# Kernel optimization log

Measured on AMD Instinct MI355X. Metric: run time of the kernel, lower is better.

Reference implementation:

```python
import jax, jax.numpy as jnp
import numpy as np

B, N, E, L = 64, 50000, 1600000, 20
BN_EPS = 1e-5


def setup_inputs() -> dict:
    key = jax.random.key(0)
    ks = jax.random.split(key, 8)
    x = jax.random.normal(ks[0], (B, N), dtype=jnp.float32)
    edge_index = jax.random.randint(ks[1], (2, E), 0, N, dtype=jnp.int32)
    alpha = jax.random.normal(ks[2], (E,), dtype=jnp.float32)
    bias = jax.random.normal(ks[3], (E,), dtype=jnp.float32)
    # LazyLinear(num_labels) on [B, N] features
    W = jax.random.normal(ks[4], (L, N), dtype=jnp.float32) / np.sqrt(N)
    b_lin = jax.random.normal(ks[5], (L,), dtype=jnp.float32) * 0.01
    # LazyBatchNorm1d affine params over N features
    gamma = jnp.ones((N,), dtype=jnp.float32)
    beta = jnp.zeros((N,), dtype=jnp.float32)
    return {"x": x, "edge_index": edge_index, "alpha": alpha, "bias": bias,
            "W": W, "b_lin": b_lin, "gamma": gamma, "beta": beta}


def reference(x, edge_index, alpha, bias, W, b_lin, gamma, beta):
    src, dst = edge_index[0], edge_index[1]
    # gather per-edge source features and apply per-edge affine: [B, E]
    x_e = alpha * x[:, src] + bias
    # scatter-mean into destination nodes: [B, N]
    sums = jnp.zeros((x.shape[0], N), dtype=x.dtype).at[:, dst].add(x_e)
    counts = jnp.zeros((N,), dtype=x.dtype).at[dst].add(1.0)
    x_hat = sums / jnp.maximum(counts, 1.0)
    out = jnp.tanh(x_hat)
    # linear head: [B, L]
    pred = x_hat @ W.T + b_lin
    # BatchNorm1d (training mode: batch stats, biased variance)
    mu = jnp.mean(out, axis=0)
    var = jnp.var(out, axis=0)
    bn = (out - mu) / jnp.sqrt(var + BN_EPS) * gamma + beta
    return (pred, bn)
```

## Files before the change

kernel.cpp:

```cpp
#include <hip/hip_runtime.h>
#include <math.h>

#define NB 64
#define NL 20
#define BN_EPS 1e-5f

#define BIN_W 32
#define NBIN 1563
#define BIN_CAP 1280
#define CHUNK 4096

#define NSB 49
#define NSBP 64
#define CAP1 36864
#define NSLICE 9

__device__ __forceinline__ unsigned short f2bf(float f) {
    unsigned u = __float_as_uint(f);
    unsigned r = u + 0x7fff + ((u >> 16) & 1);
    return (unsigned short)(r >> 16);
}

__global__ __launch_bounds__(1024) void stage_kernel(
    const float* __restrict__ x, unsigned short* __restrict__ xTb,
    const int* __restrict__ src, const int* __restrict__ dst,
    const float* __restrict__ alpha, const float* __restrict__ bias,
    int* __restrict__ cnt1, uint2* __restrict__ buf1, int E, int Nn, int nA) {
    __shared__ unsigned hist[NSBP];
    __shared__ unsigned gbase[NSBP];
    __shared__ float tile[64][65];

    int tid = threadIdx.x;

    if ((int)blockIdx.x < nA) {
        int e0 = blockIdx.x * CHUNK;
        if (tid < NSBP) hist[tid] = 0;
        __syncthreads();

        uint2 pay[4];
        unsigned rk[4];
        int sb[4];
        #pragma unroll
        for (int k = 0; k < 4; ++k) {
            int e = e0 + k * 1024 + tid;
            sb[k] = -1;
            if (e < E) {
                int d = dst[e];
                int b = d >> 5;
                int dl = d & 31;
                pay[k].x = (unsigned)src[e] | ((unsigned)f2bf(alpha[e]) << 16);
                pay[k].y = (unsigned)f2bf(bias[e]) | ((unsigned)dl << 16) |
                           ((unsigned)b << 21);
                sb[k] = d >> 10;
                rk[k] = atomicAdd(&hist[sb[k]], 1u);
            }
        }
        __syncthreads();

        if (tid < NSBP) {
            unsigned v = hist[tid];
            if (v > 0) gbase[tid] = (unsigned)atomicAdd(&cnt1[tid], (int)v);
        }
        __syncthreads();

        #pragma unroll
        for (int k = 0; k < 4; ++k) {
            if (sb[k] >= 0) {
                unsigned di = gbase[sb[k]] + rk[k];
                if (di < CAP1)
                    buf1[(size_t)sb[k] * CAP1 + di] = pay[k];
            }
        }
    } else {
        int n0 = ((int)blockIdx.x - nA) * 64;
        int ln = tid & 63;
        int wv = tid >> 6;
        for (int r = wv; r < 64; r += 16) {
            int col = n0 + ln;
            tile[r][ln] = (col < Nn) ? x[r * Nn + col] : 0.f;
        }
        __syncthreads();
        for (int r = wv; r < 64; r += 16) {
            int node = n0 + r;
            if (node < Nn) xTb[(size_t)node * 64 + ln] = f2bf(tile[ln][r]);
        }
    }
}

__global__ __launch_bounds__(1024) void binB_kernel(
    const int* __restrict__ cnt1, const uint2* __restrict__ buf1,
    int* __restrict__ cursor, uint2* __restrict__ paybins) {
    __shared__ unsigned hist[32];
    __shared__ unsigned gbase[32];

    int tid = threadIdx.x;
    int sb = blockIdx.x / NSLICE;
    int slice = blockIdx.x % NSLICE;

    int lim = cnt1[sb];
    if (lim > CAP1) lim = CAP1;
    int cc = lim - slice * 4096;
    if (cc < 0) cc = 0;
    if (cc > 4096) cc = 4096;
    const uint2* pb = buf1 + (size_t)sb * CAP1 + (size_t)slice * 4096;

    if (tid < 32) hist[tid] = 0;
    __syncthreads();

    uint2 pay[4];
    unsigned rk[4];
    int lb[4];
    #pragma unroll
    for (int k = 0; k < 4; ++k) {
        int i = k * 1024 + tid;
        lb[k] = -1;
        if (i < cc) {
            pay[k] = pb[i];
            lb[k] = (int)((pay[k].y >> 21) & 31u);
            rk[k] = atomicAdd(&hist[lb[k]], 1u);
        }
    }
    __syncthreads();

    if (tid < 32) {
        unsigned v = hist[tid];
        if (v > 0)
            gbase[tid] = (unsigned)atomicAdd(&cursor[sb * 32 + tid], (int)v);
    }
    __syncthreads();

    #pragma unroll
    for (int k = 0; k < 4; ++k) {
        if (lb[k] >= 0) {
            int bin = sb * 32 + lb[k];
            unsigned di = gbase[lb[k]] + rk[k];
            if (di < BIN_CAP)
                paybins[(size_t)bin * BIN_CAP + di] = pay[k];
        }
    }
}

__global__ __launch_bounds__(256) void pull_fin4_kernel(
    const int* __restrict__ cursor, const uint2* __restrict__ paybins,
    const unsigned short* __restrict__ xTb, const float* __restrict__ W,
    const float* __restrict__ gamma, const float* __restrict__ beta,
    float* __restrict__ pred_part, float* __restrict__ bn, int Nn) {
    __shared__ __align__(16) char smem[16896];
    uint2* ed = (uint2*)smem;
    float (*xh)[66] = (float (*)[66])smem;
    float (*th)[66] = (float (*)[66])(smem + 8448);

    __shared__ float wl[NL][32];
    __shared__ unsigned h2[32], b2[32], c2[32];
    __shared__ float mu_s[32], a_s[32], be_s[32];

    const unsigned* xTbu = (const unsigned*)xTb;

    int bin = blockIdx.x;
    int tid = threadIdx.x;
    int ln = tid & 63;
    int w = tid >> 6;
    int n0 = bin * 32;
    int pair = ln >> 5;
    int h = ln & 31;

    int cnt = cursor[bin];
    if (cnt > BIN_CAP) cnt = BIN_CAP;
    const uint2* pb = paybins + (size_t)bin * BIN_CAP;

    for (int i = tid; i < NL * 32; i += 256) {
        int l = i >> 5, j = i & 31;
        wl[l][j] = (n0 + j < Nn) ? W[l * Nn + n0 + j] : 0.f;
    }
    if (tid < 32) { h2[tid] = 0; c2[tid] = 0; }
    __syncthreads();

    uint2 pA = {0, 0}, pB = {0, 0}, pC = {0, 0}, pD = {0, 0}, pE = {0, 0};
    {
        int i;
        i = tid;
        if (i < cnt) { pA = pb[i]; atomicAdd(&h2[(pA.y >> 16) & 31], 1u); }
        i = tid + 256;
        if (i < cnt) { pB = pb[i]; atomicAdd(&h2[(pB.y >> 16) & 31], 1u); }
        i = tid + 512;
        if (i < cnt) { pC = pb[i]; atomicAdd(&h2[(pC.y >> 16) & 31], 1u); }
        i = tid + 768;
        if (i < cnt) { pD = pb[i]; atomicAdd(&h2[(pD.y >> 16) & 31], 1u); }
        i = tid + 1024;
        if (i < cnt) { pE = pb[i]; atomicAdd(&h2[(pE.y >> 16) & 31], 1u); }
    }
    __syncthreads();

    if (tid < 32) {
        unsigned v = h2[tid];
        unsigned incl = v;
        #pragma unroll
        for (int off = 1; off < 32; off <<= 1) {
            unsigned t = __shfl_up(incl, off, 64);
            if (tid >= off) incl += t;
        }
        b2[tid] = incl - v;
    }
    __syncthreads();

    {
        if (tid < cnt) {
            unsigned dl = (pA.y >> 16) & 31;
            ed[b2[dl] + atomicAdd(&c2[dl], 1u)] = pA;
        }
        if (tid + 256 < cnt) {
            unsigned dl = (pB.y >> 16) & 31;
            ed[b2[dl] + atomicAdd(&c2[dl], 1u)] = pB;
        }
        if (tid + 512 < cnt) {
            unsigned dl = (pC.y >> 16) & 31;
            ed[b2[dl] + atomicAdd(&c2[dl], 1u)] = pC;
        }
        if (tid + 768 < cnt) {
            unsigned dl = (pD.y >> 16) & 31;
            ed[b2[dl] + atomicAdd(&c2[dl], 1u)] = pD;
        }
        if (tid + 1024 < cnt) {
            unsigned dl = (pE.y >> 16) & 31;
            ed[b2[dl] + atomicAdd(&c2[dl], 1u)] = pE;
        }
    }
    __syncthreads();

    float xv_reg[8], tv_reg[8];
    #pragma unroll
    for (int k = 0; k < 8; ++k) {
        int dl = w * 8 + k;
        int node = n0 + dl;
        int n = (int)h2[dl];
        unsigned bs = b2[dl];
        float accL0 = 0.f, accH0 = 0.f, accL1 = 0.f, accH1 = 0.f;
        float bs0 = 0.f, bs1 = 0.f;
        int j = 0;
        for (; j + 3 < n; j += 4) {
            uint2 e0 = ed[bs + j + pair];
            uint2 e1 = ed[bs + j + 2 + pair];
            unsigned v0 = xTbu[(size_t)(e0.x & 0xffffu) * 32 + h];
            unsigned v1 = xTbu[(size_t)(e1.x & 0xffffu) * 32 + h];
            float al0 = __uint_as_float(e0.x & 0xffff0000u);
            float al1 = __uint_as_float(e1.x & 0xffff0000u);
            bs0 += __uint_as_float((e0.y & 0xffffu) << 16);
            bs1 += __uint_as_float((e1.y & 0xffffu) << 16);
            accL0 = fmaf(al0, __uint_as_float(v0 << 16), accL0);
            accH0 = fmaf(al0, __uint_as_float(v0 & 0xffff0000u), accH0);
            accL1 = fmaf(al1, __uint_as_float(v1 << 16), accL1);
            accH1 = fmaf(al1, __uint_as_float(v1 & 0xffff0000u), accH1);
        }
        for (; j < n; j += 2) {
            int idx = j + pair;
            bool act = idx < n;
            uint2 e0 = ed[act ? (bs + idx) : bs];
            float al0 = act ? __uint_as_float(e0.x & 0xffff0000u) : 0.f;
            float bi0 = act ? __uint_as_float((e0.y & 0xffffu) << 16) : 0.f;
            unsigned v0 = xTbu[(size_t)(e0.x & 0xffffu) * 32 + h];
            bs0 += bi0;
            accL0 = fmaf(al0, __uint_as_float(v0 << 16), accL0);
            accH0 = fmaf(al0, __uint_as_float(v0 & 0xffff0000u), accH0);
        }
        float accL = accL0 + accL1;
        float accH = accH0 + accH1;
        float bsum = bs0 + bs1;
        accL += __shfl_xor(accL, 32, 64);
        accH += __shfl_xor(accH, 32, 64);
        bsum += __shfl_xor(bsum, 32, 64);
        float inv = 1.0f / fmaxf((float)n, 1.0f);
        float xlo = (accL + bsum) * inv;
        float xhi = (accH + bsum) * inv;
        float xv = pair ? xhi : xlo;
        float tv = tanhf(xv);
        xv_reg[k] = xv;
        tv_reg[k] = tv;

        float s = tv, q = tv * tv;
        #pragma unroll
        for (int off = 32; off > 0; off >>= 1) {
            s += __shfl_xor(s, off, 64);
            q += __shfl_xor(q, off, 64);
        }
        if (ln == 0) {
            float mu = s * (1.0f / 64.0f);
            float var = fmaxf(q * (1.0f / 64.0f) - mu * mu, 0.f);
            float invs = rsqrtf(var + BN_EPS);
            float gm = 1.f, bt = 0.f;
            if (node < Nn) { gm = gamma[node]; bt = beta[node]; }
            mu_s[dl] = mu;
            a_s[dl] = invs * gm;
            be_s[dl] = bt;
        }
    }
    __syncthreads();

    {
        int col = 2 * h + pair;
        #pragma unroll
        for (int k = 0; k < 8; ++k) {
            xh[w * 8 + k][col] = xv_reg[k];
            th[w * 8 + k][col] = tv_reg[k];
        }
    }
    __syncthreads();

    {
        float acc[5] = {0.f, 0.f, 0.f, 0.f, 0.f};
        for (int n = 0; n < 32; ++n) {
            float xv = xh[n][ln];
            #pragma unroll
            for (int k = 0; k < 5; ++k)
                acc[k] = fmaf(xv, wl[w + k * 4][n], acc[k]);
        }
        #pragma unroll
        for (int k = 0; k < 5; ++k)
            pred_part[(size_t)bin * (NB * NL) + ln * NL + (w + k * 4)] = acc[k];
    }

    for (int idx = tid; idx < 32 * 64; idx += 256) {
        int noff = idx & 31, bb = idx >> 5;
        int node = n0 + noff;
        if (node < Nn)
            bn[bb * Nn + node] =
                fmaf(th[noff][bb] - mu_s[noff], a_s[noff], be_s[noff]);
    }
}

__global__ __launch_bounds__(256) void reduce_pred_kernel(
    const float* __restrict__ part, const float* __restrict__ b_lin,
    float* __restrict__ pred, int nblk) {
    int out = blockIdx.x * 4 + (threadIdx.x >> 6);
    if (out >= NB * NL) return;
    int ln = threadIdx.x & 63;
    float s = 0.f;
    for (int i = ln; i < nblk; i += 64)
        s += part[(size_t)i * (NB * NL) + out];
    #pragma unroll
    for (int off = 32; off > 0; off >>= 1)
        s += __shfl_xor(s, off, 64);
    if (ln == 0) pred[out] = b_lin[out % NL] + s;
}

extern "C" void kernel_launch(void* const* d_in, const int* in_sizes, int n_in,
                              void* d_out, int out_size, void* d_ws, size_t ws_size,
                              hipStream_t stream) {
    const float* x     = (const float*)d_in[0];
    const int*   ei    = (const int*)d_in[1];
    const float* alpha = (const float*)d_in[2];
    const float* bias  = (const float*)d_in[3];
    const float* W     = (const float*)d_in[4];
    const float* b_lin = (const float*)d_in[5];
    const float* gamma = (const float*)d_in[6];
    const float* beta  = (const float*)d_in[7];

    const int Nn = in_sizes[0] / NB;
    const int E  = in_sizes[1] / 2;
    const int* src = ei;
    const int* dst = ei + E;

    const int ntile = (Nn + 63) / 64;
    const int nA    = (E + CHUNK - 1) / CHUNK;

    uint2*          paybins = (uint2*)d_ws;
    uint2*          buf1    = paybins + (size_t)NBIN * BIN_CAP;
    float*          pred_part = (float*)buf1;
    unsigned short* xTb     = (unsigned short*)(buf1 + (size_t)NSB * CAP1);
    int*            cnt1    = (int*)(xTb + (size_t)Nn * 64);
    int*            cursor  = cnt1 + NSBP;

    float* pred = (float*)d_out;
    float* bn   = pred + NB * NL;

    hipMemsetAsync(cnt1, 0, (NSBP + NBIN + 32) * sizeof(int), stream);

    stage_kernel<<<nA + ntile, 1024, 0, stream>>>(
        x, xTb, src, dst, alpha, bias, cnt1, buf1, E, Nn, nA);
    binB_kernel<<<NSB * NSLICE, 1024, 0, stream>>>(cnt1, buf1, cursor, paybins);
    pull_fin4_kernel<<<NBIN, 256, 0, stream>>>(cursor, paybins, xTb, W,
                                               gamma, beta, pred_part, bn, Nn);
    reduce_pred_kernel<<<(NB * NL + 3) / 4, 256, 0, stream>>>(
        pred_part, b_lin, pred, NBIN);
}
```

Before: 188.9 us.

## Halve destination bin width to 16 nodes and split pred reduction in two stages

Destination bins shrink from 32 to 16 nodes, which doubles the number of pull blocks (3125) and halves each block's shared memory and edge load, so more blocks can be resident and the gather latency is spread more evenly. The bin index encoding and binB local histogram widen to 64 sub-bins per superbin to match. Because the larger number of per-bin partial pred rows makes the final reduction longer, it becomes a two-stage reduction (128 blocks, then a final pass). Bounds checks on node < Nn are dropped, which relies on N being a multiple of 16. The per-bin capacity of 640 makes overflow drops more likely if a bin is denser than expected.

```diff
diff --git a/kernel.cpp b/kernel.cpp
--- a/kernel.cpp
+++ b/kernel.cpp
@@ -5,15 +5,18 @@
 #define NL 20
 #define BN_EPS 1e-5f
 
-#define BIN_W 32
-#define NBIN 1563
-#define BIN_CAP 1280
+#define BIN_W 16
+#define NBIN 3125
+#define BIN_CAP 640
 #define CHUNK 4096
 
 #define NSB 49
 #define NSBP 64
 #define CAP1 36864
 #define NSLICE 9
+
+#define RB 128
+#define BPR 25
 
 __device__ __forceinline__ unsigned short f2bf(float f) {
     unsigned u = __float_as_uint(f);
@@ -46,11 +49,11 @@
             sb[k] = -1;
             if (e < E) {
                 int d = dst[e];
-                int b = d >> 5;
-                int dl = d & 31;
+                int b = d >> 4;
+                int dl = d & 15;
                 pay[k].x = (unsigned)src[e] | ((unsigned)f2bf(alpha[e]) << 16);
                 pay[k].y = (unsigned)f2bf(bias[e]) | ((unsigned)dl << 16) |
-                           ((unsigned)b << 21);
+                           ((unsigned)b << 20);
                 sb[k] = d >> 10;
                 rk[k] = atomicAdd(&hist[sb[k]], 1u);
             }
@@ -90,8 +93,8 @@
 __global__ __launch_bounds__(1024) void binB_kernel(
     const int* __restrict__ cnt1, const uint2* __restrict__ buf1,
     int* __restrict__ cursor, uint2* __restrict__ paybins) {
-    __shared__ unsigned hist[32];
-    __shared__ unsigned gbase[32];
+    __shared__ unsigned hist[64];
+    __shared__ unsigned gbase[64];
 
     int tid = threadIdx.x;
     int sb = blockIdx.x / NSLICE;
@@ -104,7 +107,7 @@
     if (cc > 4096) cc = 4096;
     const uint2* pb = buf1 + (size_t)sb * CAP1 + (size_t)slice * 4096;
 
-    if (tid < 32) hist[tid] = 0;
+    if (tid < 64) hist[tid] = 0;
     __syncthreads();
 
     uint2 pay[4];
@@ -116,23 +119,23 @@
         lb[k] = -1;
         if (i < cc) {
             pay[k] = pb[i];
-            lb[k] = (int)((pay[k].y >> 21) & 31u);
+            lb[k] = (int)((pay[k].y >> 20) & 63u);
             rk[k] = atomicAdd(&hist[lb[k]], 1u);
         }
     }
     __syncthreads();
 
-    if (tid < 32) {
+    if (tid < 64) {
         unsigned v = hist[tid];
         if (v > 0)
-            gbase[tid] = (unsigned)atomicAdd(&cursor[sb * 32 + tid], (int)v);
+            gbase[tid] = (unsigned)atomicAdd(&cursor[sb * 64 + tid], (int)v);
     }
     __syncthreads();
 
     #pragma unroll
     for (int k = 0; k < 4; ++k) {
         if (lb[k] >= 0) {
-            int bin = sb * 32 + lb[k];
+            int bin = sb * 64 + lb[k];
             unsigned di = gbase[lb[k]] + rk[k];
             if (di < BIN_CAP)
                 paybins[(size_t)bin * BIN_CAP + di] = pay[k];
@@ -140,19 +143,19 @@
     }
 }
 
-__global__ __launch_bounds__(256) void pull_fin4_kernel(
+__global__ __launch_bounds__(256) void pull_fin5_kernel(
     const int* __restrict__ cursor, const uint2* __restrict__ paybins,
     const unsigned short* __restrict__ xTb, const float* __restrict__ W,
     const float* __restrict__ gamma, const float* __restrict__ beta,
     float* __restrict__ pred_part, float* __restrict__ bn, int Nn) {
-    __shared__ __align__(16) char smem[16896];
+    __shared__ __align__(16) char smem[8448];
     uint2* ed = (uint2*)smem;
     float (*xh)[66] = (float (*)[66])smem;
-    float (*th)[66] = (float (*)[66])(smem + 8448);
-
-    __shared__ float wl[NL][32];
-    __shared__ unsigned h2[32], b2[32], c2[32];
-    __shared__ float mu_s[32], a_s[32], be_s[32];
+    float (*th)[66] = (float (*)[66])(smem + 4224);
+
+    __shared__ float wl[NL][16];
+    __shared__ unsigned h2[16], b2[16], c2[16];
+    __shared__ float mu_s[16], a_s[16], be_s[16];
 
     const unsigned* xTbu = (const unsigned*)xTb;
 
@@ -160,7 +163,7 @@
     int tid = threadIdx.x;
     int ln = tid & 63;
     int w = tid >> 6;
-    int n0 = bin * 32;
+    int n0 = bin * 16;
     int pair = ln >> 5;
     int h = ln & 31;
 
@@ -168,34 +171,26 @@
     if (cnt > BIN_CAP) cnt = BIN_CAP;
     const uint2* pb = paybins + (size_t)bin * BIN_CAP;
 
-    for (int i = tid; i < NL * 32; i += 256) {
-        int l = i >> 5, j = i & 31;
-        wl[l][j] = (n0 + j < Nn) ? W[l * Nn + n0 + j] : 0.f;
-    }
-    if (tid < 32) { h2[tid] = 0; c2[tid] = 0; }
-    __syncthreads();
-
-    uint2 pA = {0, 0}, pB = {0, 0}, pC = {0, 0}, pD = {0, 0}, pE = {0, 0};
+    for (int i = tid; i < NL * 16; i += 256) {
+        int l = i >> 4, j = i & 15;
+        wl[l][j] = W[l * Nn + n0 + j];
+    }
+    if (tid < 16) { h2[tid] = 0; c2[tid] = 0; }
+    __syncthreads();
+
+    uint2 pA = {0, 0}, pB = {0, 0}, pC = {0, 0};
     {
-        int i;
-        i = tid;
-        if (i < cnt) { pA = pb[i]; atomicAdd(&h2[(pA.y >> 16) & 31], 1u); }
-        i = tid + 256;
-        if (i < cnt) { pB = pb[i]; atomicAdd(&h2[(pB.y >> 16) & 31], 1u); }
-        i = tid + 512;
-        if (i < cnt) { pC = pb[i]; atomicAdd(&h2[(pC.y >> 16) & 31], 1u); }
-        i = tid + 768;
-        if (i < cnt) { pD = pb[i]; atomicAdd(&h2[(pD.y >> 16) & 31], 1u); }
-        i = tid + 1024;
-        if (i < cnt) { pE = pb[i]; atomicAdd(&h2[(pE.y >> 16) & 31], 1u); }
-    }
-    __syncthreads();
-
-    if (tid < 32) {
+        if (tid < cnt) { pA = pb[tid]; atomicAdd(&h2[(pA.y >> 16) & 15], 1u); }
+        if (tid + 256 < cnt) { pB = pb[tid + 256]; atomicAdd(&h2[(pB.y >> 16) & 15], 1u); }
+        if (tid + 512 < cnt) { pC = pb[tid + 512]; atomicAdd(&h2[(pC.y >> 16) & 15], 1u); }
+    }
+    __syncthreads();
+
+    if (tid < 16) {
         unsigned v = h2[tid];
         unsigned incl = v;
         #pragma unroll
-        for (int off = 1; off < 32; off <<= 1) {
+        for (int off = 1; off < 16; off <<= 1) {
             unsigned t = __shfl_up(incl, off, 64);
             if (tid >= off) incl += t;
         }
@@ -205,32 +200,24 @@
 
     {
         if (tid < cnt) {
-            unsigned dl = (pA.y >> 16) & 31;
+            unsigned dl = (pA.y >> 16) & 15;
             ed[b2[dl] + atomicAdd(&c2[dl], 1u)] = pA;
         }
         if (tid + 256 < cnt) {
-            unsigned dl = (pB.y >> 16) & 31;
+            unsigned dl = (pB.y >> 16) & 15;
             ed[b2[dl] + atomicAdd(&c2[dl], 1u)] = pB;
         }
         if (tid + 512 < cnt) {
-            unsigned dl = (pC.y >> 16) & 31;
+            unsigned dl = (pC.y >> 16) & 15;
             ed[b2[dl] + atomicAdd(&c2[dl], 1u)] = pC;
         }
-        if (tid + 768 < cnt) {
-            unsigned dl = (pD.y >> 16) & 31;
-            ed[b2[dl] + atomicAdd(&c2[dl], 1u)] = pD;
-        }
-        if (tid + 1024 < cnt) {
-            unsigned dl = (pE.y >> 16) & 31;
-            ed[b2[dl] + atomicAdd(&c2[dl], 1u)] = pE;
-        }
-    }
-    __syncthreads();
-
-    float xv_reg[8], tv_reg[8];
-    #pragma unroll
-    for (int k = 0; k < 8; ++k) {
-        int dl = w * 8 + k;
+    }
+    __syncthreads();
+
+    float xv_reg[4], tv_reg[4];
+    #pragma unroll
+    for (int k = 0; k < 4; ++k) {
+        int dl = w * 4 + k;
         int node = n0 + dl;
         int n = (int)h2[dl];
         unsigned bs = b2[dl];
@@ -286,11 +273,9 @@
             float mu = s * (1.0f / 64.0f);
             float var = fmaxf(q * (1.0f / 64.0f) - mu * mu, 0.f);
             float invs = rsqrtf(var + BN_EPS);
-            float gm = 1.f, bt = 0.f;
-            if (node < Nn) { gm = gamma[node]; bt = beta[node]; }
             mu_s[dl] = mu;
-            a_s[dl] = invs * gm;
-            be_s[dl] = bt;
+            a_s[dl] = invs * gamma[node];
+            be_s[dl] = beta[node];
         }
     }
     __syncthreads();
@@ -298,16 +283,17 @@
     {
         int col = 2 * h + pair;
         #pragma unroll
-        for (int k = 0; k < 8; ++k) {
-            xh[w * 8 + k][col] = xv_reg[k];
-            th[w * 8 + k][col] = tv_reg[k];
+        for (int k = 0; k < 4; ++k) {
+            xh[w * 4 + k][col] = xv_reg[k];
+            th[w * 4 + k][col] = tv_reg[k];
         }
     }
     __syncthreads();
 
     {
         float acc[5] = {0.f, 0.f, 0.f, 0.f, 0.f};
-        for (int n = 0; n < 32; ++n) {
+        #pragma unroll
+        for (int n = 0; n < 16; ++n) {
             float xv = xh[n][ln];
             #pragma unroll
             for (int k = 0; k < 5; ++k)
@@ -318,16 +304,32 @@
             pred_part[(size_t)bin * (NB * NL) + ln * NL + (w + k * 4)] = acc[k];
     }
 
-    for (int idx = tid; idx < 32 * 64; idx += 256) {
-        int noff = idx & 31, bb = idx >> 5;
-        int node = n0 + noff;
-        if (node < Nn)
-            bn[bb * Nn + node] =
-                fmaf(th[noff][bb] - mu_s[noff], a_s[noff], be_s[noff]);
-    }
-}
-
-__global__ __launch_bounds__(256) void reduce_pred_kernel(
+    for (int idx = tid; idx < 16 * 64; idx += 256) {
+        int noff = idx & 15, bb = idx >> 4;
+        bn[bb * Nn + n0 + noff] =
+            fmaf(th[noff][bb] - mu_s[noff], a_s[noff], be_s[noff]);
+    }
+}
+
+__global__ __launch_bounds__(256) void reduce1_kernel(
+    const float* __restrict__ part, float* __restrict__ out2, int nbin) {
+    int r = blockIdx.x;
+    int b0 = r * BPR;
+    int b1 = b0 + BPR;
+    if (b1 > nbin) b1 = nbin;
+    float acc[5] = {0.f, 0.f, 0.f, 0.f, 0.f};
+    for (int b = b0; b < b1; ++b) {
+        const float* p = part + (size_t)b * (NB * NL);
+        #pragma unroll
+        for (int k = 0; k < 5; ++k)
+            acc[k] += p[threadIdx.x + k * 256];
+    }
+    #pragma unroll
+    for (int k = 0; k < 5; ++k)
+        out2[(size_t)r * (NB * NL) + threadIdx.x + k * 256] = acc[k];
+}
+
+__global__ __launch_bounds__(256) void reduce2_kernel(
     const float* __restrict__ part, const float* __restrict__ b_lin,
     float* __restrict__ pred, int nblk) {
     int out = blockIdx.x * 4 + (threadIdx.x >> 6);
@@ -365,20 +367,22 @@
     uint2*          paybins = (uint2*)d_ws;
     uint2*          buf1    = paybins + (size_t)NBIN * BIN_CAP;
     float*          pred_part = (float*)buf1;
-    unsigned short* xTb     = (unsigned short*)(buf1 + (size_t)NSB * CAP1);
+    char*           ubuf_end = (char*)buf1 + (size_t)NBIN * NB * NL * 4;
+    unsigned short* xTb     = (unsigned short*)ubuf_end;
     int*            cnt1    = (int*)(xTb + (size_t)Nn * 64);
     int*            cursor  = cnt1 + NSBP;
+    float*          out2    = (float*)(cursor + NSB * 64);
 
     float* pred = (float*)d_out;
     float* bn   = pred + NB * NL;
 
-    hipMemsetAsync(cnt1, 0, (NSBP + NBIN + 32) * sizeof(int), stream);
+    hipMemsetAsync(cnt1, 0, (NSBP + NSB * 64) * sizeof(int), stream);
 
     stage_kernel<<<nA + ntile, 1024, 0, stream>>>(
         x, xTb, src, dst, alpha, bias, cnt1, buf1, E, Nn, nA);
     binB_kernel<<<NSB * NSLICE, 1024, 0, stream>>>(cnt1, buf1, cursor, paybins);
-    pull_fin4_kernel<<<NBIN, 256, 0, stream>>>(cursor, paybins, xTb, W,
+    pull_fin5_kernel<<<NBIN, 256, 0, stream>>>(cursor, paybins, xTb, W,
                                                gamma, beta, pred_part, bn, Nn);
-    reduce_pred_kernel<<<(NB * NL + 3) / 4, 256, 0, stream>>>(
-        pred_part, b_lin, pred, NBIN);
-}
+    reduce1_kernel<<<RB, 256, 0, stream>>>(pred_part, out2, NBIN);
+    reduce2_kernel<<<(NB * NL + 3) / 4, 256, 0, stream>>>(out2, b_lin, pred, RB);
+}
```

New measurement: 184.0 us. -2.6%, faster.
